# Performance work log

Hardware: AMD Instinct MI355X
Metric: run time of the kernel (lower is better)

## Reference

```python
import jax, jax.numpy as jnp
import numpy as np

NEG_SLOPE = 0.1
NUM_HEADS = 16
ATT0, ATT1 = 64, 64
FOCUS = 3

def lrelu(x):
    return jnp.where(x >= 0, x, NEG_SLOPE * x)

def adaptive_pool_sum(x, a0, a1):
    # adaptive max pool + adaptive avg pool (exact windows since h%a0==0, w%a1==0)
    B, C, h, w = x.shape
    f0, f1 = h // a0, w // a1
    xr = x.reshape(B, C, a0, f0, a1, f1)
    return xr.max(axis=(3, 5)) + xr.mean(axis=(3, 5))

def upsample_bilinear_ac(x, H, W):
    # bilinear upsample with align_corners=True, matching nn.Upsample
    B, C, h, w = x.shape
    def grid(n_out, n_in):
        t = jnp.arange(n_out, dtype=x.dtype) * ((n_in - 1) / (n_out - 1))
        i0 = jnp.clip(jnp.floor(t).astype(jnp.int32), 0, n_in - 2)
        return i0, t - i0.astype(x.dtype)
    y0, wy = grid(H, h)
    x0, wx = grid(W, w)
    wy = wy[None, None, :, None]
    r = x[:, :, y0, :] * (1 - wy) + x[:, :, y0 + 1, :] * wy
    return r[:, :, :, x0] * (1 - wx) + r[:, :, :, x0 + 1] * wx

def _forward(input1, input2, w_in, b_in, w_v, b_v, scale_param, pos1, pos2):
    B, C, W, H = input1.shape
    N = ATT0 * ATT1
    HD = C // NUM_HEADS
    # conv2input: 1x1 conv dim//2 -> dim (channels differ)
    input2 = jnp.einsum('oc,bchw->bohw', w_in, input2) + b_in[None, :, None, None]
    p1 = adaptive_pool_sum(input1, ATT0, ATT1)  # (B,C,64,64)
    p2 = adaptive_pool_sum(input2, ATT0, ATT1)
    q = p1.reshape(B, C, N).transpose(0, 2, 1)  # (B,N,C)
    t2 = p2.reshape(B, C, N).transpose(0, 2, 1)
    q = lrelu(q + pos1)
    k = lrelu(t2 + pos2)
    v = t2
    scale = jax.nn.softplus(scale_param)  # (1,1,C)
    q = q / scale
    k = k / scale
    def focus(t):
        n = jnp.linalg.norm(t, axis=-1, keepdims=True)
        tp = t ** FOCUS
        return n / jnp.linalg.norm(tp, axis=-1, keepdims=True) * tp
    q = focus(q)
    k = focus(k)
    # head split is head-major: C -> (num_heads, head_dim)
    qh = q.reshape(B, N, NUM_HEADS, HD).transpose(0, 2, 1, 3)  # (B,h,N,d)
    kh = k.reshape(B, N, NUM_HEADS, HD).transpose(0, 2, 1, 3)
    vh = v.reshape(B, N, NUM_HEADS, HD).transpose(0, 2, 1, 3)
    # kv-first linear attention: (k^T N^-.5) @ (v N^-.5) = k^T v / N
    kv = jnp.einsum('bhnd,bhne->bhde', kh, vh) / N  # (B,h,d,d)
    x = jnp.einsum('bhnd,bhde->bhne', qh, kv)       # (B,h,N,d)
    x = x.transpose(0, 1, 3, 2).reshape(B, C, N)     # (B,h,d,N) -> (B,C,N)
    # per-head 1x1 conv + leaky relu on v
    v4 = vh.reshape(B * NUM_HEADS, ATT0, ATT1, HD)
    vc = lrelu(jnp.einsum('bxyd,od->boxy', v4, w_v) + b_v[None, :, None, None])
    x = x + vc.reshape(B, C, N)
    attn = x.reshape(B, C, ATT0, ATT1)
    attn = upsample_bilinear_ac(attn, W, H)
    return jax.nn.sigmoid(attn)

def setup_inputs():
    key = jax.random.key(0)
    ks = jax.random.split(key, 6)
    dim, half, hd, N = 512, 256, 32, ATT0 * ATT1
    return {
        'input1': jax.random.normal(ks[0], (8, dim, 128, 128), jnp.float32),
        'input2': jax.random.normal(ks[1], (8, half, 128, 128), jnp.float32),
        'w_in': jax.random.normal(ks[2], (dim, half), jnp.float32) * 0.05,
        'b_in': jnp.zeros((dim,), jnp.float32),
        'w_v': jax.random.normal(ks[3], (hd, hd), jnp.float32) * 0.1,
        'b_v': jnp.zeros((hd,), jnp.float32),
        'scale_param': jnp.zeros((1, 1, dim), jnp.float32),  # nn.Parameter init zeros
        'pos1': jax.random.normal(ks[4], (1, N, dim), jnp.float32) * 0.02,
        'pos2': jax.random.normal(ks[5], (1, N, dim), jnp.float32) * 0.02,
    }

def reference(input1, input2, w_in, b_in, w_v, b_v, scale_param, pos1, pos2):
    return _forward(input1, input2, w_in, b_in, w_v, b_v, scale_param, pos1, pos2)
```

## Files before the change

### kernel.cpp

```cpp
#include <hip/hip_runtime.h>
#include <hip/hip_bf16.h>
#include <math.h>

#define NEG 0.1f

typedef __attribute__((ext_vector_type(8))) short short8;
typedef __attribute__((ext_vector_type(4))) float f32x4;

__device__ __forceinline__ float lrelu(float x){ return x >= 0.f ? x : NEG*x; }

__device__ __forceinline__ unsigned pk2(float lo, float hi){
    __hip_bfloat162 h = __float22bfloat162_rn(make_float2(lo, hi));
    union { __hip_bfloat162 h2; unsigned u; } cv; cv.h2 = h;
    return cv.u;
}
__device__ __forceinline__ float bflo(unsigned u){ return __uint_as_float(u << 16); }
__device__ __forceinline__ float bfhi(unsigned u){ return __uint_as_float(u & 0xFFFF0000u); }

__global__ __launch_bounds__(256) void k_wprep(const float* __restrict__ w_in, unsigned* __restrict__ wbf_u){
    int idx8 = (blockIdx.x*256 + threadIdx.x)*8;
    float4 v0 = *(const float4*)&w_in[idx8];
    float4 v1 = *(const float4*)&w_in[idx8+4];
    uint4 d;
    d.x = pk2(v0.x, v0.y); d.y = pk2(v0.z, v0.w);
    d.z = pk2(v1.x, v1.y); d.w = pk2(v1.z, v1.w);
    *(uint4*)&wbf_u[idx8>>1] = d;
}

__global__ __launch_bounds__(256) void k_pool1(const float* __restrict__ in1, unsigned* __restrict__ p1u){
    const int y = blockIdx.x, cg = blockIdx.y, b = blockIdx.z;
    const int tid = threadIdx.x;
    const int x = tid & 63, w = tid >> 6;
    const int cbase = cg*32 + w*8;
    const float2* iv = (const float2*)in1;
    float out[8];
    #pragma unroll
    for (int j = 0; j < 8; ++j){
        int c = cbase + j;
        size_t r0 = (size_t)(b*512 + c)*8192 + (2*y)*64 + x;
        float2 a = iv[r0];
        float2 bb = iv[r0 + 64];
        float m = fmaxf(fmaxf(a.x,a.y), fmaxf(bb.x,bb.y));
        out[j] = m + (a.x+a.y+bb.x+bb.y)*0.25f;
    }
    uint4 d;
    d.x = pk2(out[0],out[1]); d.y = pk2(out[2],out[3]);
    d.z = pk2(out[4],out[5]); d.w = pk2(out[6],out[7]);
    int n = y*64 + x;
    *(uint4*)&p1u[(size_t)(b*4096 + n)*256 + cg*16 + w*4] = d;
}

__global__ __launch_bounds__(256) void k_convpool(const float* __restrict__ in2, const unsigned* __restrict__ wbf_u,
                                                  const float* __restrict__ b_in, unsigned short* __restrict__ p2t){
    __shared__ unsigned As[128*33];
    __shared__ unsigned Bs[128*32];
    const int b = blockIdx.z, o0 = blockIdx.y*128;
    const int y = blockIdx.x >> 1, xg = blockIdx.x & 1;
    const int tid = threadIdx.x;
    const int lane = tid & 63, w = tid >> 6;
    const int col = lane & 15, q = lane >> 4;

    f32x4 acc[2][8];
    #pragma unroll
    for (int mt=0; mt<2; ++mt)
        #pragma unroll
        for (int nt=0; nt<8; ++nt) acc[mt][nt] = (f32x4){0.f,0.f,0.f,0.f};

    const int a_o8 = tid >> 3;
    const int a_kg = tid & 7;
    const int b_c4 = tid & 15, b_r = (tid>>4)&1, b_kg = tid>>5;
    const int b_n = b_r*64 + b_c4*4;

    for (int kb = 0; kb < 4; ++kb){
        __syncthreads();
        #pragma unroll
        for (int pass=0; pass<4; ++pass){
            int o = pass*32 + a_o8;
            uint4 d = *(const uint4*)&wbf_u[((size_t)(o0+o)*256 + kb*64 + a_kg*8) >> 1];
            *(uint4*)&As[o*32 + ((a_kg ^ ((o>>1)&7))<<2)] = d;
        }
        float r[8][4];
        #pragma unroll
        for (int kk=0; kk<8; ++kk){
            int k = kb*64 + b_kg*8 + kk;
            float4 v = *(const float4*)&in2[((size_t)(b*256 + k)*128 + 2*y + b_r)*128 + xg*64 + b_c4*4];
            r[kk][0]=v.x; r[kk][1]=v.y; r[kk][2]=v.z; r[kk][3]=v.w;
        }
        #pragma unroll
        for (int i=0; i<4; ++i){
            int n = b_n + i;
            uint4 d;
            d.x = pk2(r[0][i], r[1][i]); d.y = pk2(r[2][i], r[3][i]);
            d.z = pk2(r[4][i], r[5][i]); d.w = pk2(r[6][i], r[7][i]);
            *(uint4*)&Bs[n*32 + ((b_kg ^ ((n>>1)&7))<<2)] = d;
        }
        __syncthreads();
        #pragma unroll
        for (int ks=0; ks<2; ++ks){
            int g = ks*4 + q;
            short8 af[2], bf[8];
            #pragma unroll
            for (int mt=0; mt<2; ++mt){
                int m = w*32 + mt*16 + col;
                af[mt] = *(const short8*)&As[m*32 + ((g ^ ((m>>1)&7))<<2)];
            }
            #pragma unroll
            for (int nt=0; nt<8; ++nt){
                int n = nt*16 + col;
                bf[nt] = *(const short8*)&Bs[n*32 + ((g ^ ((n>>1)&7))<<2)];
            }
            #pragma unroll
            for (int mt=0; mt<2; ++mt)
                #pragma unroll
                for (int nt=0; nt<8; ++nt)
                    acc[mt][nt] = __builtin_amdgcn_mfma_f32_16x16x32_bf16(af[mt], bf[nt], acc[mt][nt], 0,0,0);
        }
    }
    __syncthreads();
    float* outs = (float*)As;
    #pragma unroll
    for (int mt=0; mt<2; ++mt){
        #pragma unroll
        for (int nt=0; nt<4; ++nt){
            #pragma unroll
            for (int reg=0; reg<4; ++reg){
                float a = acc[mt][nt][reg], bb = acc[mt][nt+4][reg];
                float mx = fmaxf(a, bb), sm = a + bb;
                float mx2 = fmaxf(mx, __shfl_xor(mx, 1));
                float sm2 = sm + __shfl_xor(sm, 1);
                if ((lane & 1) == 0){
                    int p = nt*8 + (col>>1);
                    int o = w*32 + mt*16 + q*4 + reg;
                    outs[o*33 + p] = mx2 + sm2*0.25f;
                }
            }
        }
    }
    __syncthreads();
    const int o4 = tid & 31, pp = tid >> 5;
    #pragma unroll
    for (int pass=0; pass<4; ++pass){
        int p = pass*8 + pp;
        int n = y*64 + xg*32 + p;
        float v0 = outs[(o4*4+0)*33 + p] + 2.0f*b_in[o0+o4*4+0];
        float v1 = outs[(o4*4+1)*33 + p] + 2.0f*b_in[o0+o4*4+1];
        float v2 = outs[(o4*4+2)*33 + p] + 2.0f*b_in[o0+o4*4+2];
        float v3 = outs[(o4*4+3)*33 + p] + 2.0f*b_in[o0+o4*4+3];
        uint2 d; d.x = pk2(v0,v1); d.y = pk2(v2,v3);
        *(uint2*)&p2t[(size_t)(b*4096 + n)*512 + o0 + o4*4] = d;
    }
}

__global__ __launch_bounds__(256) void k_rows(unsigned* __restrict__ p1u, const unsigned* __restrict__ p2u,
                                              const float* __restrict__ pos1, const float* __restrict__ pos2,
                                              const float* __restrict__ scale_param, unsigned* __restrict__ kfu){
    const int b = blockIdx.y;
    const int tid = threadIdx.x;
    const int half = tid >> 7, t = tid & 127;
    const int n = blockIdx.x*2 + half;
    const int c0 = t*4;
    const size_t base2 = (size_t)(b*4096 + n)*128;
    __shared__ float red[4][4];
    uint2 u1 = *(const uint2*)&p1u[base2*2 + t*2];
    uint2 u2 = *(const uint2*)&p2u[base2*2 + t*2];
    float4 po1 = *(const float4*)&pos1[n*512 + c0];
    float4 po2 = *(const float4*)&pos2[n*512 + c0];
    float4 scv = *(const float4*)&scale_param[c0];
    float qv[4], kv_[4];
    float pq2=0.f, pq6=0.f, pk2_=0.f, pk6=0.f;
    {
        float p1a[4] = {bflo(u1.x), bfhi(u1.x), bflo(u1.y), bfhi(u1.y)};
        float p2a[4] = {bflo(u2.x), bfhi(u2.x), bflo(u2.y), bfhi(u2.y)};
        float poa1[4] = {po1.x,po1.y,po1.z,po1.w};
        float poa2[4] = {po2.x,po2.y,po2.z,po2.w};
        float sca[4] = {scv.x,scv.y,scv.z,scv.w};
        #pragma unroll
        for (int j = 0; j < 4; ++j){
            float sp = sca[j];
            float inv = 1.0f/(fmaxf(sp,0.f) + log1pf(expf(-fabsf(sp))));
            float qq = lrelu(p1a[j] + poa1[j]) * inv;
            float kk = lrelu(p2a[j] + poa2[j]) * inv;
            qv[j]=qq; kv_[j]=kk;
            float a;
            a = qq*qq; pq2 += a; pq6 += a*a*a;
            a = kk*kk; pk2_ += a; pk6 += a*a*a;
        }
    }
    #pragma unroll
    for (int off = 32; off > 0; off >>= 1){
        pq2 += __shfl_xor(pq2, off);
        pq6 += __shfl_xor(pq6, off);
        pk2_ += __shfl_xor(pk2_, off);
        pk6 += __shfl_xor(pk6, off);
    }
    int wave = tid >> 6;
    if ((tid & 63) == 0){ red[wave][0]=pq2; red[wave][1]=pq6; red[wave][2]=pk2_; red[wave][3]=pk6; }
    __syncthreads();
    float sq2 = red[2*half][0]+red[2*half+1][0];
    float sq6 = red[2*half][1]+red[2*half+1][1];
    float sk2 = red[2*half][2]+red[2*half+1][2];
    float sk6 = red[2*half][3]+red[2*half+1][3];
    float fq = sqrtf(sq2/sq6);
    float fk = sqrtf(sk2/sk6);
    uint2 dq, dk;
    dq.x = pk2(qv[0]*qv[0]*qv[0]*fq, qv[1]*qv[1]*qv[1]*fq);
    dq.y = pk2(qv[2]*qv[2]*qv[2]*fq, qv[3]*qv[3]*qv[3]*fq);
    dk.x = pk2(kv_[0]*kv_[0]*kv_[0]*fk, kv_[1]*kv_[1]*kv_[1]*fk);
    dk.y = pk2(kv_[2]*kv_[2]*kv_[2]*fk, kv_[3]*kv_[3]*kv_[3]*fk);
    *(uint2*)&p1u[base2*2 + t*2] = dq;
    *(uint2*)&kfu[base2*2 + t*2] = dk;
}

__global__ __launch_bounds__(256) void k_kv(const unsigned* __restrict__ kfu, const unsigned* __restrict__ p2u,
                                            float* __restrict__ kv){
    __shared__ unsigned ksu[4096], vsu[4096];
    const int nc = blockIdx.x, h = blockIdx.y, b = blockIdx.z;
    const int tid = threadIdx.x;
    #pragma unroll
    for (int it = 0; it < 16; ++it){
        int i = it*256 + tid;
        int n = i >> 4, u = i & 15;
        size_t g = (size_t)(b*4096 + nc*256 + n)*256 + h*16 + u;
        ksu[i] = kfu[g];
        vsu[i] = p2u[g];
    }
    __syncthreads();
    const int d = tid >> 3, e2 = (tid & 7)*2;
    const unsigned kmaskhi = (d & 1) ? 1u : 0u;
    float acc[4] = {0.f,0.f,0.f,0.f};
    #pragma unroll 8
    for (int n = 0; n < 256; ++n){
        unsigned ku = ksu[n*16 + (d>>1)];
        float kd = kmaskhi ? bfhi(ku) : bflo(ku);
        uint2 vv = *(const uint2*)&vsu[n*16 + e2];
        acc[0] += kd*bflo(vv.x); acc[1] += kd*bfhi(vv.x);
        acc[2] += kd*bflo(vv.y); acc[3] += kd*bfhi(vv.y);
    }
    float* dst = &kv[((size_t)(b*16 + h)*32 + d)*32 + (tid&7)*4];
    const float sc = 1.0f/4096.0f;
    atomicAdd(dst+0, acc[0]*sc);
    atomicAdd(dst+1, acc[1]*sc);
    atomicAdd(dst+2, acc[2]*sc);
    atomicAdd(dst+3, acc[3]*sc);
}

__global__ __launch_bounds__(256) void k_attn(const unsigned* __restrict__ qfu, const unsigned* __restrict__ p2u,
                                              const float* __restrict__ kv, const float* __restrict__ w_v,
                                              const float* __restrict__ b_v, unsigned short* __restrict__ attn){
    __shared__ float kvs[1024];
    __shared__ float wvsT[32*36];
    __shared__ float qsl[64*32];
    __shared__ float vsl[64*32];
    __shared__ float to[32*66];
    const int nt = blockIdx.x, h = blockIdx.y, b = blockIdx.z;
    const int tid = threadIdx.x;
    #pragma unroll
    for (int it = 0; it < 4; ++it){
        int i = it*256 + tid;
        kvs[i] = kv[(size_t)(b*16 + h)*1024 + i];
        int e_ = i >> 5, d_ = i & 31;
        wvsT[d_*36 + e_] = w_v[e_*32 + d_];
    }
    #pragma unroll
    for (int it = 0; it < 4; ++it){
        int i = it*256 + tid;
        int nn = i >> 4, cp = i & 15;
        size_t g = (size_t)(b*4096 + nt*64 + nn)*256 + h*16 + cp;
        unsigned qu = qfu[g], vu = p2u[g];
        qsl[nn*32 + cp*2]   = bflo(qu);
        qsl[nn*32 + cp*2+1] = bfhi(qu);
        vsl[nn*32 + cp*2]   = bflo(vu);
        vsl[nn*32 + cp*2+1] = bfhi(vu);
    }
    __syncthreads();
    const int e0 = (tid & 7)*4, ng = tid >> 3;
    float4 bv = make_float4(b_v[e0], b_v[e0+1], b_v[e0+2], b_v[e0+3]);
    #pragma unroll
    for (int half = 0; half < 2; ++half){
        int nn = ng + half*32;
        float xa[4] = {0.f,0.f,0.f,0.f}, va[4] = {0.f,0.f,0.f,0.f};
        #pragma unroll
        for (int dq = 0; dq < 8; ++dq){
            float4 q4 = *(const float4*)&qsl[nn*32 + dq*4];
            float4 v4 = *(const float4*)&vsl[nn*32 + dq*4];
            float qarr[4] = {q4.x,q4.y,q4.z,q4.w};
            float varr[4] = {v4.x,v4.y,v4.z,v4.w};
            #pragma unroll
            for (int l = 0; l < 4; ++l){
                int d = dq*4 + l;
                float4 kvv = *(const float4*)&kvs[d*32 + e0];
                float4 wvv = *(const float4*)&wvsT[d*36 + e0];
                xa[0] += qarr[l]*kvv.x; xa[1] += qarr[l]*kvv.y; xa[2] += qarr[l]*kvv.z; xa[3] += qarr[l]*kvv.w;
                va[0] += varr[l]*wvv.x; va[1] += varr[l]*wvv.y; va[2] += varr[l]*wvv.z; va[3] += varr[l]*wvv.w;
            }
        }
        to[(e0+0)*66 + nn] = xa[0] + lrelu(va[0] + bv.x);
        to[(e0+1)*66 + nn] = xa[1] + lrelu(va[1] + bv.y);
        to[(e0+2)*66 + nn] = xa[2] + lrelu(va[2] + bv.z);
        to[(e0+3)*66 + nn] = xa[3] + lrelu(va[3] + bv.w);
    }
    __syncthreads();
    const int cc = tid >> 3, n0 = (tid & 7)*8;
    uint4 d;
    d.x = pk2(to[cc*66+n0+0], to[cc*66+n0+1]);
    d.y = pk2(to[cc*66+n0+2], to[cc*66+n0+3]);
    d.z = pk2(to[cc*66+n0+4], to[cc*66+n0+5]);
    d.w = pk2(to[cc*66+n0+6], to[cc*66+n0+7]);
    *(uint4*)&attn[((size_t)(b*512) + h*32 + cc)*4096 + nt*64 + n0] = d;
}

__global__ __launch_bounds__(256) void k_up(const unsigned* __restrict__ attn_u, float* __restrict__ out){
    __shared__ float sA[18*65];
    const int qy = blockIdx.x;
    const int bc = blockIdx.y;
    const int tid = threadIdx.x;
    const int ybase = (qy*32*63)/127;
    const size_t sb = (size_t)bc*2048;
    for (int i = tid; i < 576; i += 256){
        int r = i >> 5, cu = i & 31;
        int ridx = ybase + r; if (ridx > 63) ridx = 63;
        unsigned u = attn_u[sb + ridx*32 + cu];
        sA[r*65 + cu*2]   = bflo(u);
        sA[r*65 + cu*2+1] = bfhi(u);
    }
    __syncthreads();
    const float rr = 63.0f/127.0f;
    const int ro = tid >> 3, cbase = tid & 7;
    const int yo = qy*32 + ro;
    float ty = yo * rr;
    int y0 = (int)ty; y0 = y0 > 62 ? 62 : y0;
    float wy = ty - (float)y0;
    const float* ra = &sA[(y0 - ybase)*65];
    const float* rb = ra + 65;
    float* orow = &out[((size_t)bc*128 + yo)*128];
    #pragma unroll
    for (int t = 0; t < 4; ++t){
        int xo0 = (cbase + t*8)*4;
        float4 o;
        float* op = (float*)&o;
        #pragma unroll
        for (int j = 0; j < 4; ++j){
            int xo = xo0 + j;
            float tx = xo * rr;
            int x0 = (int)tx; x0 = x0 > 62 ? 62 : x0;
            float wx = tx - (float)x0;
            float a00 = ra[x0], a01 = ra[x0+1];
            float a10 = rb[x0], a11 = rb[x0+1];
            float v = (a00*(1.f-wy) + a10*wy)*(1.f-wx) + (a01*(1.f-wy) + a11*wy)*wx;
            op[j] = 1.0f/(1.0f + expf(-v));
        }
        *(float4*)&orow[xo0] = o;
    }
}

extern "C" void kernel_launch(void* const* d_in, const int* in_sizes, int n_in,
                              void* d_out, int out_size, void* d_ws, size_t ws_size,
                              hipStream_t stream){
    const float* in1  = (const float*)d_in[0];
    const float* in2  = (const float*)d_in[1];
    const float* w_in = (const float*)d_in[2];
    const float* b_in = (const float*)d_in[3];
    const float* w_v  = (const float*)d_in[4];
    const float* b_v  = (const float*)d_in[5];
    const float* scp  = (const float*)d_in[6];
    const float* pos1 = (const float*)d_in[7];
    const float* pos2 = (const float*)d_in[8];
    float* out = (float*)d_out;
    char* ws  = (char*)d_ws;

    const size_t PBYTES = (size_t)8*4096*512*2;
    unsigned short* p1t  = (unsigned short*)ws;
    unsigned short* p2t  = (unsigned short*)(ws + PBYTES);
    unsigned short* kfoc = (unsigned short*)(ws + 2*PBYTES);
    float*          kvb  = (float*)(ws + 3*PBYTES);
    unsigned*       wbf  = (unsigned*)(ws + 3*PBYTES + (size_t)8*16*32*32*4);

    hipMemsetAsync(kvb, 0, (size_t)8*16*32*32*sizeof(float), stream);
    k_wprep   <<<64,            256, 0, stream>>>(w_in, wbf);
    k_pool1   <<<dim3(64,16,8), 256, 0, stream>>>(in1, (unsigned*)p1t);
    k_convpool<<<dim3(128,4,8), 256, 0, stream>>>(in2, wbf, b_in, p2t);
    k_rows    <<<dim3(2048,8),  256, 0, stream>>>((unsigned*)p1t, (const unsigned*)p2t, pos1, pos2, scp, (unsigned*)kfoc);
    k_kv      <<<dim3(16,16,8), 256, 0, stream>>>((const unsigned*)kfoc, (const unsigned*)p2t, kvb);
    k_attn    <<<dim3(64,16,8), 256, 0, stream>>>((const unsigned*)p1t, (const unsigned*)p2t, kvb, w_v, b_v, kfoc);
    k_up      <<<dim3(4,4096),  256, 0, stream>>>((const unsigned*)kfoc, out);
}
```

Before: 813.6 us.

## Stage input2 tile once per block and loop over all output channels in convpool

The 1x1 conv + pool kernel now loads a 2x64-pixel strip of input2 (all 256 channels) into shared memory once, converts it to bf16, and then iterates over the four 128-channel output groups internally. Previously each of four output-channel blocks reread and reconverted the same input2 data. This cuts global reads of the large fp32 input by about 4x. In exchange each block has a smaller N tile (64 pixels), more LDS (48KB), and fewer blocks (2048 vs 4096), which may lower occupancy and MFMA reuse per A-tile load.

```diff
diff --git a/kernel.cpp b/kernel.cpp
--- a/kernel.cpp
+++ b/kernel.cpp
@@ -51,103 +51,107 @@
 }
 
 __global__ __launch_bounds__(256) void k_convpool(const float* __restrict__ in2, const unsigned* __restrict__ wbf_u,
-                                                  const float* __restrict__ b_in, unsigned short* __restrict__ p2t){
-    __shared__ unsigned As[128*33];
-    __shared__ unsigned Bs[128*32];
-    const int b = blockIdx.z, o0 = blockIdx.y*128;
-    const int y = blockIdx.x >> 1, xg = blockIdx.x & 1;
+                                                  const float* __restrict__ b_in, unsigned* __restrict__ p2u){
+    __shared__ unsigned Bs[64*128];
+    __shared__ unsigned As[128*32];
+    const int b = blockIdx.y;
+    const int Y = blockIdx.x >> 2, X = blockIdx.x & 3;
     const int tid = threadIdx.x;
     const int lane = tid & 63, w = tid >> 6;
     const int col = lane & 15, q = lane >> 4;
 
-    f32x4 acc[2][8];
-    #pragma unroll
-    for (int mt=0; mt<2; ++mt)
-        #pragma unroll
-        for (int nt=0; nt<8; ++nt) acc[mt][nt] = (f32x4){0.f,0.f,0.f,0.f};
-
-    const int a_o8 = tid >> 3;
-    const int a_kg = tid & 7;
-    const int b_c4 = tid & 15, b_r = (tid>>4)&1, b_kg = tid>>5;
-    const int b_n = b_r*64 + b_c4*4;
-
-    for (int kb = 0; kb < 4; ++kb){
+    {
+        const int c8 = tid & 7, r = (tid>>3) & 1, kg = tid >> 4;
+        #pragma unroll
+        for (int j = 0; j < 2; ++j){
+            float v[8][4];
+            #pragma unroll
+            for (int kk = 0; kk < 8; ++kk){
+                int k = kg*16 + j*8 + kk;
+                float4 t = *(const float4*)&in2[((size_t)(b*256 + k)*128 + 2*Y + r)*128 + X*32 + c8*4];
+                v[kk][0]=t.x; v[kk][1]=t.y; v[kk][2]=t.z; v[kk][3]=t.w;
+            }
+            int g = kg*2 + j;
+            #pragma unroll
+            for (int i = 0; i < 4; ++i){
+                int px = r*32 + c8*4 + i;
+                uint4 d;
+                d.x = pk2(v[0][i], v[1][i]); d.y = pk2(v[2][i], v[3][i]);
+                d.z = pk2(v[4][i], v[5][i]); d.w = pk2(v[6][i], v[7][i]);
+                *(uint4*)&Bs[px*128 + ((g ^ (px & 7)) << 2)] = d;
+            }
+        }
+    }
+
+    const int a_o8 = tid >> 3, a_kg = tid & 7;
+    const int u6 = tid & 63, pq = tid >> 6;
+
+    for (int o0 = 0; o0 < 4; ++o0){
+        f32x4 acc[2][4];
+        #pragma unroll
+        for (int mt=0; mt<2; ++mt)
+            #pragma unroll
+            for (int nt=0; nt<4; ++nt) acc[mt][nt] = (f32x4){0.f,0.f,0.f,0.f};
+
+        for (int kb = 0; kb < 4; ++kb){
+            __syncthreads();
+            #pragma unroll
+            for (int pass=0; pass<4; ++pass){
+                int o = pass*32 + a_o8;
+                uint4 d = *(const uint4*)&wbf_u[((size_t)(o0*128+o)*256 + kb*64 + a_kg*8) >> 1];
+                *(uint4*)&As[o*32 + ((a_kg ^ ((o>>1)&7))<<2)] = d;
+            }
+            __syncthreads();
+            #pragma unroll
+            for (int ks=0; ks<2; ++ks){
+                short8 af[2], bf[4];
+                #pragma unroll
+                for (int mt=0; mt<2; ++mt){
+                    int m = w*32 + mt*16 + col;
+                    af[mt] = *(const short8*)&As[m*32 + (((ks*4+q) ^ ((m>>1)&7))<<2)];
+                }
+                int g = kb*8 + ks*4 + q;
+                #pragma unroll
+                for (int nt=0; nt<4; ++nt){
+                    int px = nt*16 + col;
+                    bf[nt] = *(const short8*)&Bs[px*128 + ((g ^ (px & 7))<<2)];
+                }
+                #pragma unroll
+                for (int mt=0; mt<2; ++mt)
+                    #pragma unroll
+                    for (int nt=0; nt<4; ++nt)
+                        acc[mt][nt] = __builtin_amdgcn_mfma_f32_16x16x32_bf16(af[mt], bf[nt], acc[mt][nt], 0,0,0);
+            }
+        }
         __syncthreads();
-        #pragma unroll
-        for (int pass=0; pass<4; ++pass){
-            int o = pass*32 + a_o8;
-            uint4 d = *(const uint4*)&wbf_u[((size_t)(o0+o)*256 + kb*64 + a_kg*8) >> 1];
-            *(uint4*)&As[o*32 + ((a_kg ^ ((o>>1)&7))<<2)] = d;
-        }
-        float r[8][4];
-        #pragma unroll
-        for (int kk=0; kk<8; ++kk){
-            int k = kb*64 + b_kg*8 + kk;
-            float4 v = *(const float4*)&in2[((size_t)(b*256 + k)*128 + 2*y + b_r)*128 + xg*64 + b_c4*4];
-            r[kk][0]=v.x; r[kk][1]=v.y; r[kk][2]=v.z; r[kk][3]=v.w;
-        }
-        #pragma unroll
-        for (int i=0; i<4; ++i){
-            int n = b_n + i;
-            uint4 d;
-            d.x = pk2(r[0][i], r[1][i]); d.y = pk2(r[2][i], r[3][i]);
-            d.z = pk2(r[4][i], r[5][i]); d.w = pk2(r[6][i], r[7][i]);
-            *(uint4*)&Bs[n*32 + ((b_kg ^ ((n>>1)&7))<<2)] = d;
+        float* outs = (float*)As;
+        #pragma unroll
+        for (int mt=0; mt<2; ++mt){
+            #pragma unroll
+            for (int ntp=0; ntp<2; ++ntp){
+                #pragma unroll
+                for (int reg=0; reg<4; ++reg){
+                    float a = acc[mt][ntp][reg], bb = acc[mt][ntp+2][reg];
+                    float mx = fmaxf(a, bb), sm = a + bb;
+                    float mx2 = fmaxf(mx, __shfl_xor(mx, 1));
+                    float sm2 = sm + __shfl_xor(sm, 1);
+                    if ((lane & 1) == 0){
+                        int p = ntp*8 + (col>>1);
+                        int o = w*32 + mt*16 + q*4 + reg;
+                        outs[o*17 + p] = mx2 + sm2*0.25f;
+                    }
+                }
+            }
         }
         __syncthreads();
         #pragma unroll
-        for (int ks=0; ks<2; ++ks){
-            int g = ks*4 + q;
-            short8 af[2], bf[8];
-            #pragma unroll
-            for (int mt=0; mt<2; ++mt){
-                int m = w*32 + mt*16 + col;
-                af[mt] = *(const short8*)&As[m*32 + ((g ^ ((m>>1)&7))<<2)];
-            }
-            #pragma unroll
-            for (int nt=0; nt<8; ++nt){
-                int n = nt*16 + col;
-                bf[nt] = *(const short8*)&Bs[n*32 + ((g ^ ((n>>1)&7))<<2)];
-            }
-            #pragma unroll
-            for (int mt=0; mt<2; ++mt)
-                #pragma unroll
-                for (int nt=0; nt<8; ++nt)
-                    acc[mt][nt] = __builtin_amdgcn_mfma_f32_16x16x32_bf16(af[mt], bf[nt], acc[mt][nt], 0,0,0);
-        }
-    }
-    __syncthreads();
-    float* outs = (float*)As;
-    #pragma unroll
-    for (int mt=0; mt<2; ++mt){
-        #pragma unroll
-        for (int nt=0; nt<4; ++nt){
-            #pragma unroll
-            for (int reg=0; reg<4; ++reg){
-                float a = acc[mt][nt][reg], bb = acc[mt][nt+4][reg];
-                float mx = fmaxf(a, bb), sm = a + bb;
-                float mx2 = fmaxf(mx, __shfl_xor(mx, 1));
-                float sm2 = sm + __shfl_xor(sm, 1);
-                if ((lane & 1) == 0){
-                    int p = nt*8 + (col>>1);
-                    int o = w*32 + mt*16 + q*4 + reg;
-                    outs[o*33 + p] = mx2 + sm2*0.25f;
-                }
-            }
-        }
-    }
-    __syncthreads();
-    const int o4 = tid & 31, pp = tid >> 5;
-    #pragma unroll
-    for (int pass=0; pass<4; ++pass){
-        int p = pass*8 + pp;
-        int n = y*64 + xg*32 + p;
-        float v0 = outs[(o4*4+0)*33 + p] + 2.0f*b_in[o0+o4*4+0];
-        float v1 = outs[(o4*4+1)*33 + p] + 2.0f*b_in[o0+o4*4+1];
-        float v2 = outs[(o4*4+2)*33 + p] + 2.0f*b_in[o0+o4*4+2];
-        float v3 = outs[(o4*4+3)*33 + p] + 2.0f*b_in[o0+o4*4+3];
-        uint2 d; d.x = pk2(v0,v1); d.y = pk2(v2,v3);
-        *(uint2*)&p2t[(size_t)(b*4096 + n)*512 + o0 + o4*4] = d;
+        for (int i = 0; i < 4; ++i){
+            int p = pq*4 + i;
+            int n = Y*64 + X*16 + p;
+            float vlo = outs[(u6*2  )*17 + p] + 2.0f*b_in[o0*128 + u6*2];
+            float vhi = outs[(u6*2+1)*17 + p] + 2.0f*b_in[o0*128 + u6*2+1];
+            p2u[(size_t)(b*4096 + n)*256 + o0*64 + u6] = pk2(vlo, vhi);
+        }
     }
 }
 
@@ -378,7 +382,7 @@
     hipMemsetAsync(kvb, 0, (size_t)8*16*32*32*sizeof(float), stream);
     k_wprep   <<<64,            256, 0, stream>>>(w_in, wbf);
     k_pool1   <<<dim3(64,16,8), 256, 0, stream>>>(in1, (unsigned*)p1t);
-    k_convpool<<<dim3(128,4,8), 256, 0, stream>>>(in2, wbf, b_in, p2t);
+    k_convpool<<<dim3(256,8),   256, 0, stream>>>(in2, wbf, b_in, (unsigned*)p2t);
     k_rows    <<<dim3(2048,8),  256, 0, stream>>>((unsigned*)p1t, (const unsigned*)p2t, pos1, pos2, scp, (unsigned*)kfoc);
     k_kv      <<<dim3(16,16,8), 256, 0, stream>>>((const unsigned*)kfoc, (const unsigned*)p2t, kvb);
     k_attn    <<<dim3(64,16,8), 256, 0, stream>>>((const unsigned*)p1t, (const unsigned*)p2t, kvb, w_v, b_v, kfoc);
```

Result: no change. 825.1 us (+1.4%).
